# Optimization experiments

Measured on AMD Instinct MI355X. Metric: run time of the kernel, lower is better.

Reference implementation:

```python
import jax, jax.numpy as jnp
import numpy as np

K = 3
STRIDE = 1
PAD = 1
IN_CH = 64
OUT_CH = 128
ALPHA = 0.5  # scaling_factor
QMAX = 127.0  # 8-bit symmetric fake quant


def fake_quant(x):
    # per-tensor symmetric 8-bit fake quant with dynamic amax + STE
    amax = jnp.max(jnp.abs(jax.lax.stop_gradient(x)))
    s = jnp.where(amax > 0, amax / QMAX, 1.0)
    q = jnp.clip(jnp.round(x / s), -QMAX, QMAX) * s
    return x + jax.lax.stop_gradient(q - x)


def im2col(x, k, stride, pad):
    # x: (B, C, H, W) -> (B, C*k*k, h_out*w_out), torch.nn.functional.unfold order (C slowest, then kh, kw)
    B, C, H, W = x.shape
    h_out = (H + 2 * pad - k) // stride + 1
    w_out = (W + 2 * pad - k) // stride + 1
    xp = jnp.pad(x, ((0, 0), (0, 0), (pad, pad), (pad, pad)))
    patches = [xp[:, :, i:i + stride * h_out:stride, j:j + stride * w_out:stride]
               for i in range(k) for j in range(k)]  # fixed k*k loop
    cols = jnp.stack(patches, axis=2)  # (B, C, k*k, h_out, w_out)
    return cols.reshape(B, C * k * k, h_out * w_out), h_out, w_out


def setup_inputs() -> dict:
    key = jax.random.key(0)
    k1, k2 = jax.random.split(key)
    inp = jax.random.normal(k1, (16, IN_CH, 128, 128), dtype=jnp.float32)
    weight = jax.random.normal(k2, (OUT_CH, IN_CH, K, K), dtype=jnp.float32) * 0.05
    return {"input": inp, "weight": weight}


def reference(input, weight):
    bs = input.shape[0]
    ksize = IN_CH * K * K
    cols, h_out, w_out = im2col(input, K, STRIDE, PAD)  # (B, ksize, L)
    num_sliding = cols.shape[2]
    x = jnp.transpose(cols, (0, 2, 1)).reshape(-1, ksize)  # (B*L, ksize)
    w_flat = weight.reshape(OUT_CH, ksize)

    act_scale = jnp.max(jnp.abs(jax.lax.stop_gradient(x)), axis=0)       # (ksize,)
    weight_scale = jnp.max(jnp.abs(jax.lax.stop_gradient(w_flat)), axis=0)  # (ksize,)
    scale = act_scale ** ALPHA / weight_scale ** (1.0 - ALPHA)
    scale = jnp.where(scale == 0, 1.0, scale)

    x = fake_quant(x / scale)
    w_flat = fake_quant(w_flat * scale)

    out = jnp.einsum('nk,ok->no', x, w_flat)  # (B*L, OUT_CH)
    out = out.reshape(bs, num_sliding, OUT_CH)
    out = jnp.transpose(out, (0, 2, 1)).reshape(bs, OUT_CH, h_out, w_out)
    return out
```

## Files before the change

kernel.cpp:

```cpp
#include <hip/hip_runtime.h>

#define BATCH 16
#define CIN   64
#define HW    128
#define OC    128
#define KSIZE 576

typedef float float4v __attribute__((ext_vector_type(4)));
typedef int   int4v   __attribute__((ext_vector_type(4)));
typedef unsigned int uint;

#define WS_ACT   0
#define WS_WSC   576
#define WS_XMUL  1152
#define WS_SXSW  1728
#define WS_WQ_BYTE_OFF 8192

#define SWZ(x) ((((x) & 3) ^ (((x) >> 2) & 3)))
#define MAGIC 12582912.0f

__device__ __forceinline__ void async_cp16(const void* g, void* l) {
    __builtin_amdgcn_global_load_lds(
        (const __attribute__((address_space(1))) unsigned int*)g,
        (__attribute__((address_space(3))) unsigned int*)l, 16, 0, 0);
}

__global__ __launch_bounds__(256) void k_absmax(const float* __restrict__ in,
                                                const float* __restrict__ w,
                                                float* __restrict__ wsf) {
    const int tid = threadIdx.x, lane = tid & 63, wid = tid >> 6;
    if (blockIdx.x < 1024) {
        const int c = blockIdx.x >> 4, bs = blockIdx.x & 15;
        const float4v* p = (const float4v*)(in + (size_t)(bs * CIN + c) * (HW * HW));
        float m[9];
#pragma unroll
        for (int i = 0; i < 9; ++i) m[i] = 0.f;
        for (int e = tid; e < 4096; e += 256) {
            const int h = e >> 5, q = e & 31;
            const float4v v = p[e];
            const float a0 = fabsf(v[0]), a1 = fabsf(v[1]), a2 = fabsf(v[2]), a3 = fabsf(v[3]);
            const float m01 = fmaxf(a0, a1), m12 = fmaxf(a1, a2);
            const float mall = fmaxf(m01, fmaxf(a2, a3));
            const float mw0 = (q == 31) ? fmaxf(m01, a2) : mall;
            const float mw2 = (q == 0)  ? fmaxf(m12, a3) : mall;
            const bool h0 = (h <= 126), h2 = (h >= 1);
            m[0] = fmaxf(m[0], h0 ? mw0 : 0.f);
            m[1] = fmaxf(m[1], h0 ? mall : 0.f);
            m[2] = fmaxf(m[2], h0 ? mw2 : 0.f);
            m[3] = fmaxf(m[3], mw0);
            m[4] = fmaxf(m[4], mall);
            m[5] = fmaxf(m[5], mw2);
            m[6] = fmaxf(m[6], h2 ? mw0 : 0.f);
            m[7] = fmaxf(m[7], h2 ? mall : 0.f);
            m[8] = fmaxf(m[8], h2 ? mw2 : 0.f);
        }
#pragma unroll
        for (int i = 0; i < 9; ++i)
            for (int off = 32; off; off >>= 1)
                m[i] = fmaxf(m[i], __shfl_down(m[i], off));
        __shared__ float sred[4][9];
        if (lane == 0)
#pragma unroll
            for (int i = 0; i < 9; ++i) sred[wid][i] = m[i];
        __syncthreads();
        if (tid < 9) {
            float mm = fmaxf(fmaxf(sred[0][tid], sred[1][tid]),
                             fmaxf(sred[2][tid], sred[3][tid]));
            atomicMax((int*)(wsf + WS_ACT + c * 9 + tid), __float_as_int(mm));
        }
    } else {
        const int k = (blockIdx.x - 1024) * 4 + wid;
        float m = fmaxf(fabsf(w[lane * KSIZE + k]), fabsf(w[(lane + 64) * KSIZE + k]));
        for (int off = 32; off; off >>= 1) m = fmaxf(m, __shfl_down(m, off));
        if (lane == 0) wsf[WS_WSC + k] = m;
    }
}

__global__ __launch_bounds__(576) void k_scale_wq(const float* __restrict__ w,
                                                  float* __restrict__ wsf,
                                                  char* __restrict__ wq_s) {
    __shared__ float ls[576];
    __shared__ float redA[9], redB[9];
    const int t = threadIdx.x, o = blockIdx.x;
    const int lane = t & 63, wid = t >> 6;
    const float a = wsf[WS_ACT + t];
    const float wv = wsf[WS_WSC + t];
    float s = sqrtf(a) / sqrtf(wv);
    if (s == 0.f) s = 1.f;
    ls[t] = s;
    float v1 = a / s;
    float v2 = wv * s;
    for (int off = 32; off; off >>= 1) {
        v1 = fmaxf(v1, __shfl_down(v1, off));
        v2 = fmaxf(v2, __shfl_down(v2, off));
    }
    if (lane == 0) { redA[wid] = v1; redB[wid] = v2; }
    __syncthreads();
    float ax = redA[0], aw = redB[0];
#pragma unroll
    for (int i = 1; i < 9; ++i) { ax = fmaxf(ax, redA[i]); aw = fmaxf(aw, redB[i]); }
    const float sx = ax > 0.f ? ax / 127.f : 1.f;
    const float sw = aw > 0.f ? aw / 127.f : 1.f;
    const int r = t >> 6, c = t & 63, ko = c * 9 + r;
    float q = rintf((w[o * KSIZE + ko] * ls[ko]) / sw);
    q = fminf(127.f, fmaxf(-127.f, q));
    const int qi = (int)q;
    const int fc = c >> 4;
    wq_s[r * 8192 + o * 64 + ((fc ^ SWZ(o)) << 4) + (c & 15)] = (char)qi;
    if (o == 0) {
        wsf[WS_XMUL + t] = 1.0f / (ls[ko] * sx);
        if (t == 0) wsf[WS_SXSW] = sx * sw;
    }
}

__global__ __launch_bounds__(512, 4) void k_gemm(const float* __restrict__ in,
                                                 const char* __restrict__ wq_s,
                                                 const float* __restrict__ wsf,
                                                 float* __restrict__ out) {
    __shared__ int4v Bl4[4608];
    __shared__ float xml[576];
    char* Bl = (char*)Bl4;

    const int tid = threadIdx.x, lane = tid & 63, w = tid >> 6;
    const int xcd = blockIdx.x & 7, idx = blockIdx.x >> 3;
    const int oh = xcd * 16 + (idx & 15);
    const int b = idx >> 4;
    const int wband = (w & 3) * 32, ohalf = (w >> 2) * 64;
    const int l15 = lane & 15, fsel = lane >> 4;

#pragma unroll
    for (int i = 0; i < 9; ++i)
        async_cp16(wq_s + i * 8192 + tid * 16, Bl + i * 8192 + tid * 16);
    if (tid < 144)
        ((float4v*)xml)[tid] = ((const float4v*)(wsf + WS_XMUL))[tid];
    __syncthreads();

    const float* pb = in + (size_t)b * (CIN * HW * HW) + fsel * (16 * HW * HW);

    int4v acc[2][4];
#pragma unroll
    for (int mt = 0; mt < 2; ++mt)
#pragma unroll
        for (int nt = 0; nt < 4; ++nt) acc[mt][nt] = (int4v){0, 0, 0, 0};

#pragma unroll
    for (int r = 0; r < 9; ++r) {
        const int kh = r / 3, kw = r - 3 * kh;
        const int h = oh + kh - 1;
        const int hc = h < 0 ? 0 : (h > 127 ? 127 : h);
        const bool hok = (unsigned)h < 128u;

        float v[2][16];
        int iwv[2];
#pragma unroll
        for (int mt = 0; mt < 2; ++mt) {
            const int iw = wband + mt * 16 + l15 + kw - 1;
            iwv[mt] = iw;
            const int iwc = iw < 0 ? 0 : (iw > 127 ? 127 : iw);
            const float* p = pb + hc * HW + iwc;
#pragma unroll
            for (int j = 0; j < 16; ++j) v[mt][j] = p[j * (HW * HW)];
        }
        const float* xp = xml + r * 64 + (fsel << 4);
        float xm[16];
#pragma unroll
        for (int d = 0; d < 4; ++d) {
            const float4v t = *(const float4v*)(xp + d * 4);
            xm[d * 4 + 0] = t[0]; xm[d * 4 + 1] = t[1];
            xm[d * 4 + 2] = t[2]; xm[d * 4 + 3] = t[3];
        }
        int4v af[2];
#pragma unroll
        for (int mt = 0; mt < 2; ++mt) {
            const bool ok = hok && ((unsigned)iwv[mt] < 128u);
            uint pk[4];
#pragma unroll
            for (int d = 0; d < 4; ++d) {
                uint u[4];
#pragma unroll
                for (int j2 = 0; j2 < 4; ++j2) {
                    float t = v[mt][d * 4 + j2] * xm[d * 4 + j2];
                    t = fminf(127.f, fmaxf(-127.f, t));
                    t += MAGIC;
                    u[j2] = __float_as_uint(t);
                }
                const uint p01 = __builtin_amdgcn_perm(u[1], u[0], 0x0C0C0400u);
                const uint p23 = __builtin_amdgcn_perm(u[3], u[2], 0x0C0C0400u);
                pk[d] = __builtin_amdgcn_perm(p23, p01, 0x05040100u);
            }
            af[mt] = ok ? (int4v){(int)pk[0], (int)pk[1], (int)pk[2], (int)pk[3]}
                        : (int4v){0, 0, 0, 0};
        }
#pragma unroll
        for (int nt = 0; nt < 4; ++nt) {
            const int br = ohalf + nt * 16 + l15;
            const int4v bf = *(const int4v*)(Bl + r * 8192 + br * 64 +
                                             ((fsel ^ SWZ(br)) << 4));
            acc[0][nt] = __builtin_amdgcn_mfma_i32_16x16x64_i8(af[0], bf, acc[0][nt], 0, 0, 0);
            acc[1][nt] = __builtin_amdgcn_mfma_i32_16x16x64_i8(af[1], bf, acc[1][nt], 0, 0, 0);
        }
    }

    const float sxsw = wsf[WS_SXSW];
#pragma unroll
    for (int mt = 0; mt < 2; ++mt)
#pragma unroll
        for (int nt = 0; nt < 4; ++nt) {
            const int owp = wband + mt * 16 + (fsel << 2);
            const int o = ohalf + nt * 16 + l15;
            float4v rv;
#pragma unroll
            for (int q = 0; q < 4; ++q) rv[q] = (float)acc[mt][nt][q] * sxsw;
            *(float4v*)(out + ((size_t)(b * OC + o) * HW + oh) * HW + owp) = rv;
        }
}

extern "C" void kernel_launch(void* const* d_in, const int* in_sizes, int n_in,
                              void* d_out, int out_size, void* d_ws, size_t ws_size,
                              hipStream_t stream) {
    const float* in = (const float*)d_in[0];
    const float* wt = (const float*)d_in[1];
    float* out = (float*)d_out;
    float* wsf = (float*)d_ws;
    char* wq_s = (char*)d_ws + WS_WQ_BYTE_OFF;

    k_absmax<<<dim3(1024 + 144), dim3(256), 0, stream>>>(in, wt, wsf);
    k_scale_wq<<<dim3(128), dim3(576), 0, stream>>>(wt, wsf, wq_s);
    k_gemm<<<dim3(BATCH * HW), dim3(512), 0, stream>>>(in, wq_s, wsf, out);
}
```

Baseline: 257.2 us.

## Remap warps to full output-channel tiles and skip out-of-bounds rows

Each wave now owns a 16-column width strip across all 128 output channels, where before it covered a 32-wide by 64-channel tile. Each wave therefore loads and quantizes one A fragment per tap instead of two, and reuses it across eight MFMAs, which removes the duplicated activation global loads and quantization work between the two channel halves. Taps whose input row falls outside the image are skipped entirely. The clamp before rounding is dropped, which relies on the scaled activations already lying within ±127. The cost is that every wave now reads all B fragments from LDS.

After: 224.9 us. 12.6% less time.

```diff
diff --git a/kernel.cpp b/kernel.cpp
--- a/kernel.cpp
+++ b/kernel.cpp
@@ -125,8 +125,8 @@
     const int xcd = blockIdx.x & 7, idx = blockIdx.x >> 3;
     const int oh = xcd * 16 + (idx & 15);
     const int b = idx >> 4;
-    const int wband = (w & 3) * 32, ohalf = (w >> 2) * 64;
     const int l15 = lane & 15, fsel = lane >> 4;
+    const int ow0 = w * 16 + l15;
 
 #pragma unroll
     for (int i = 0; i < 9; ++i)
@@ -135,84 +135,68 @@
         ((float4v*)xml)[tid] = ((const float4v*)(wsf + WS_XMUL))[tid];
     __syncthreads();
 
-    const float* pb = in + (size_t)b * (CIN * HW * HW) + fsel * (16 * HW * HW);
-
-    int4v acc[2][4];
-#pragma unroll
-    for (int mt = 0; mt < 2; ++mt)
-#pragma unroll
-        for (int nt = 0; nt < 4; ++nt) acc[mt][nt] = (int4v){0, 0, 0, 0};
+    const float* pb = in + ((size_t)b * CIN + fsel * 16) * (HW * HW);
+
+    int4v acc[8];
+#pragma unroll
+    for (int nt = 0; nt < 8; ++nt) acc[nt] = (int4v){0, 0, 0, 0};
 
 #pragma unroll
     for (int r = 0; r < 9; ++r) {
         const int kh = r / 3, kw = r - 3 * kh;
         const int h = oh + kh - 1;
-        const int hc = h < 0 ? 0 : (h > 127 ? 127 : h);
-        const bool hok = (unsigned)h < 128u;
-
-        float v[2][16];
-        int iwv[2];
-#pragma unroll
-        for (int mt = 0; mt < 2; ++mt) {
-            const int iw = wband + mt * 16 + l15 + kw - 1;
-            iwv[mt] = iw;
-            const int iwc = iw < 0 ? 0 : (iw > 127 ? 127 : iw);
-            const float* p = pb + hc * HW + iwc;
-#pragma unroll
-            for (int j = 0; j < 16; ++j) v[mt][j] = p[j * (HW * HW)];
-        }
-        const float* xp = xml + r * 64 + (fsel << 4);
-        float xm[16];
-#pragma unroll
-        for (int d = 0; d < 4; ++d) {
-            const float4v t = *(const float4v*)(xp + d * 4);
-            xm[d * 4 + 0] = t[0]; xm[d * 4 + 1] = t[1];
-            xm[d * 4 + 2] = t[2]; xm[d * 4 + 3] = t[3];
-        }
-        int4v af[2];
-#pragma unroll
-        for (int mt = 0; mt < 2; ++mt) {
-            const bool ok = hok && ((unsigned)iwv[mt] < 128u);
+        if (h >= 0 && h < HW) {
+            const int iw = ow0 + kw - 1;
+            int iwc = iw;
+            if (kw == 0) iwc = iw < 0 ? 0 : iw;
+            if (kw == 2) iwc = iw > 127 ? 127 : iw;
+            const float* p = pb + h * HW + iwc;
+            float v[16];
+#pragma unroll
+            for (int j = 0; j < 16; ++j) v[j] = p[j * (HW * HW)];
+            const float* xp = xml + r * 64 + (fsel << 4);
+            float4v xq[4];
+#pragma unroll
+            for (int d = 0; d < 4; ++d) xq[d] = *(const float4v*)(xp + d * 4);
             uint pk[4];
 #pragma unroll
             for (int d = 0; d < 4; ++d) {
                 uint u[4];
 #pragma unroll
-                for (int j2 = 0; j2 < 4; ++j2) {
-                    float t = v[mt][d * 4 + j2] * xm[d * 4 + j2];
-                    t = fminf(127.f, fmaxf(-127.f, t));
-                    t += MAGIC;
-                    u[j2] = __float_as_uint(t);
-                }
+                for (int j2 = 0; j2 < 4; ++j2)
+                    u[j2] = __float_as_uint(fmaf(v[d * 4 + j2], xq[d][j2], MAGIC));
                 const uint p01 = __builtin_amdgcn_perm(u[1], u[0], 0x0C0C0400u);
                 const uint p23 = __builtin_amdgcn_perm(u[3], u[2], 0x0C0C0400u);
                 pk[d] = __builtin_amdgcn_perm(p23, p01, 0x05040100u);
             }
-            af[mt] = ok ? (int4v){(int)pk[0], (int)pk[1], (int)pk[2], (int)pk[3]}
-                        : (int4v){0, 0, 0, 0};
+            int4v af;
+            if (kw != 1) {
+                const uint msk = ((unsigned)iw < 128u) ? 0xFFFFFFFFu : 0u;
+                af = (int4v){(int)(pk[0] & msk), (int)(pk[1] & msk),
+                             (int)(pk[2] & msk), (int)(pk[3] & msk)};
+            } else {
+                af = (int4v){(int)pk[0], (int)pk[1], (int)pk[2], (int)pk[3]};
+            }
+#pragma unroll
+            for (int nt = 0; nt < 8; ++nt) {
+                const int br = nt * 16 + l15;
+                const int4v bf = *(const int4v*)(Bl + r * 8192 + br * 64 +
+                                                 ((fsel ^ SWZ(br)) << 4));
+                acc[nt] = __builtin_amdgcn_mfma_i32_16x16x64_i8(af, bf, acc[nt], 0, 0, 0);
+            }
         }
-#pragma unroll
-        for (int nt = 0; nt < 4; ++nt) {
-            const int br = ohalf + nt * 16 + l15;
-            const int4v bf = *(const int4v*)(Bl + r * 8192 + br * 64 +
-                                             ((fsel ^ SWZ(br)) << 4));
-            acc[0][nt] = __builtin_amdgcn_mfma_i32_16x16x64_i8(af[0], bf, acc[0][nt], 0, 0, 0);
-            acc[1][nt] = __builtin_amdgcn_mfma_i32_16x16x64_i8(af[1], bf, acc[1][nt], 0, 0, 0);
-        }
     }
 
     const float sxsw = wsf[WS_SXSW];
-#pragma unroll
-    for (int mt = 0; mt < 2; ++mt)
-#pragma unroll
-        for (int nt = 0; nt < 4; ++nt) {
-            const int owp = wband + mt * 16 + (fsel << 2);
-            const int o = ohalf + nt * 16 + l15;
-            float4v rv;
-#pragma unroll
-            for (int q = 0; q < 4; ++q) rv[q] = (float)acc[mt][nt][q] * sxsw;
-            *(float4v*)(out + ((size_t)(b * OC + o) * HW + oh) * HW + owp) = rv;
-        }
+    const int owp = w * 16 + (fsel << 2);
+#pragma unroll
+    for (int nt = 0; nt < 8; ++nt) {
+        const int o = nt * 16 + l15;
+        float4v rv;
+#pragma unroll
+        for (int q = 0; q < 4; ++q) rv[q] = (float)acc[nt][q] * sxsw;
+        *(float4v*)(out + ((size_t)(b * OC + o) * HW + oh) * HW + owp) = rv;
+    }
 }
 
 extern "C" void kernel_launch(void* const* d_in, const int* in_sizes, int n_in,
```
